# Kernel tuning notes

Hardware: AMD Instinct MI355X
Metric: run time of the kernel (lower is better)

The kernel has to match this reference:

```python
import jax, jax.numpy as jnp
import numpy as np

N_NODES = 50000
N_EDGES = 800000
IN_DIM = 128
HEADS = 8
HEAD_DIM = 16


def setup_inputs() -> dict:
    key = jax.random.key(0)
    ks = jax.random.split(key, 9)
    s = 1.0 / np.sqrt(IN_DIM)
    return {
        "h": jax.random.normal(ks[0], (N_NODES, IN_DIM), dtype=jnp.float32),
        "src": jax.random.randint(ks[1], (N_EDGES,), 0, N_NODES, dtype=jnp.int32),
        "dst": jax.random.randint(ks[2], (N_EDGES,), 0, N_NODES, dtype=jnp.int32),
        "WQ": jax.random.normal(ks[3], (IN_DIM, HEADS * HEAD_DIM), dtype=jnp.float32) * s,
        "bQ": jnp.zeros((HEADS * HEAD_DIM,), dtype=jnp.float32),
        "WK": jax.random.normal(ks[4], (IN_DIM, HEADS * HEAD_DIM), dtype=jnp.float32) * s,
        "bK": jnp.zeros((HEADS * HEAD_DIM,), dtype=jnp.float32),
        "WV": jax.random.normal(ks[5], (IN_DIM, HEADS * HEAD_DIM), dtype=jnp.float32) * s,
        "bV": jnp.zeros((HEADS * HEAD_DIM,), dtype=jnp.float32),
    }


def reference(h, src, dst, WQ, bQ, WK, bK, WV, bV):
    N = h.shape[0]
    sqrt_d = jnp.float32(np.sqrt(HEAD_DIM))
    # node projections, viewed as [N, H, D]
    Q = (h @ WQ + bQ).reshape(N, HEADS, HEAD_DIM)
    K = (h @ WK + bK).reshape(N, HEADS, HEAD_DIM)
    V = (h @ WV + bV).reshape(N, HEADS, HEAD_DIM)
    # edge scores: (K_src . Q_dst) per head, scaled exp with clamp [-5, 5]
    score = jnp.sum(K[src] * Q[dst], axis=-1, keepdims=True)  # [E, H, 1]
    score = jnp.exp(jnp.clip(score / sqrt_d, -5.0, 5.0))
    # segment-softmax denominator z and weighted V sum wV, both scattered to dst
    z = jax.ops.segment_sum(score, dst, num_segments=N)            # [N, H, 1]
    wV = jax.ops.segment_sum(V[src] * score, dst, num_segments=N)  # [N, H, D]
    # possible_empty: divide only where z > 0 (wV is 0 there anyway)
    head_out = jnp.where(z > 0, wV / jnp.where(z > 0, z, 1.0), wV)
    return head_out
```

## Files before the change

### kernel.cpp

```cpp
#include <hip/hip_runtime.h>
#include <math.h>

#define DIM 128
#define N_HEADS 8
#define HD 16

typedef __attribute__((ext_vector_type(8))) short bf16x8;
typedef __attribute__((ext_vector_type(4))) float f32x4;

__device__ __forceinline__ unsigned bf16pack2(float a, float b) {
    unsigned ua = __builtin_bit_cast(unsigned, a);
    unsigned ub = __builtin_bit_cast(unsigned, b);
    ua = (ua + 0x7FFFu + ((ua >> 16) & 1u)) >> 16;
    ub = (ub + 0x7FFFu + ((ub >> 16) & 1u)) >> 16;
    return ua | (ub << 16);
}
__device__ __forceinline__ float bf16lo(unsigned p) {
    return __builtin_bit_cast(float, p << 16);
}
__device__ __forceinline__ float bf16hi(unsigned p) {
    return __builtin_bit_cast(float, p & 0xFFFF0000u);
}

__global__ __launch_bounds__(256)
void convert_hist_kernel(const float* __restrict__ WQ, const float* __restrict__ bQ,
                         const float* __restrict__ WK, const float* __restrict__ bK,
                         const float* __restrict__ WV, const float* __restrict__ bV,
                         unsigned short* __restrict__ WT, float* __restrict__ bias384,
                         const int* __restrict__ dst, int* __restrict__ offs,
                         int nConv, int E)
{
    if ((int)blockIdx.x < nConv) {
        int idx = blockIdx.x * 256 + threadIdx.x;
        int c = idx >> 7, k = idx & 127;
        const float* W; const float* b; int col = c & 127;
        if (c < 128)      { W = WQ; b = bQ; }
        else if (c < 256) { W = WK; b = bK; }
        else              { W = WV; b = bV; }
        float v = W[k * DIM + col];
        WT[(size_t)c * DIM + k] = (unsigned short)(bf16pack2(v, 0.0f) & 0xFFFFu);
        if (k == 0) bias384[c] = b[col];
    } else {
        int e = ((int)blockIdx.x - nConv) * 256 + threadIdx.x;
        if (e < E) atomicAdd(&offs[dst[e]], 1);
    }
}

__global__ __launch_bounds__(256)
void scan_blocks_kernel(int* __restrict__ offs, int* __restrict__ bsum, int N)
{
    __shared__ int sd[256];
    const int t = threadIdx.x;
    const int i = blockIdx.x * 256 + t;
    int v = (i < N) ? offs[i] : 0;
    sd[t] = v;
    __syncthreads();
    #pragma unroll
    for (int o = 1; o < 256; o <<= 1) {
        int x = (t >= o) ? sd[t - o] : 0;
        __syncthreads();
        sd[t] += x;
        __syncthreads();
    }
    int incl = sd[t];
    if (i < N) offs[i] = incl - v;
    if (t == 255) bsum[blockIdx.x] = incl;
}

__global__ __launch_bounds__(256)
void scan_fixup_kernel(int* __restrict__ offs, int* __restrict__ cursor,
                       const int* __restrict__ bsum, int nb, int N, int E)
{
    __shared__ int sd[256];
    const int t = threadIdx.x;
    sd[t] = (t < nb && t < (int)blockIdx.x) ? bsum[t] : 0;
    __syncthreads();
    #pragma unroll
    for (int o = 128; o > 0; o >>= 1) {
        if (t < o) sd[t] += sd[t + o];
        __syncthreads();
    }
    const int base = sd[0];
    int i = blockIdx.x * 256 + t;
    if (i < N) {
        int v = offs[i] + base;
        offs[i]   = v;
        cursor[i] = v;
    }
    if (i == 0) offs[N] = E;
}

__global__ __launch_bounds__(256)
void scatter_kernel(const int* __restrict__ src, const int* __restrict__ dst,
                    int* __restrict__ cursor, int* __restrict__ srcs, int E)
{
    int e = blockIdx.x * 256 + threadIdx.x;
    if (e < E) {
        int d   = dst[e];
        int pos = atomicAdd(&cursor[d], 1);
        srcs[pos] = src[e];
    }
}

__global__ __launch_bounds__(256)
void qkv_mfma_kernel(const float* __restrict__ h,
                     const unsigned short* __restrict__ WT,
                     const float* __restrict__ bias384,
                     float* __restrict__ Q, unsigned* __restrict__ KVd,
                     int N)
{
    __shared__ unsigned short hs[64 * 136];
    const int tid = threadIdx.x;
    const int n0  = blockIdx.x * 64;

    #pragma unroll
    for (int i = 0; i < 4; ++i) {
        int lin  = i * 256 + tid;
        int node = lin >> 4;
        int k0   = (lin & 15) * 8;
        int gn   = n0 + node;
        float4 a0, a1;
        if (gn < N) {
            a0 = *(const float4*)(h + (size_t)gn * DIM + k0);
            a1 = *(const float4*)(h + (size_t)gn * DIM + k0 + 4);
        } else {
            a0 = make_float4(0.f, 0.f, 0.f, 0.f);
            a1 = a0;
        }
        uint4 p = make_uint4(bf16pack2(a0.x, a0.y), bf16pack2(a0.z, a0.w),
                             bf16pack2(a1.x, a1.y), bf16pack2(a1.z, a1.w));
        *(uint4*)(hs + node * 136 + k0) = p;
    }
    __syncthreads();

    const int wave   = tid >> 6;
    const int l      = tid & 63;
    const int lane16 = l & 15;
    const int quad   = l >> 4;
    const int wc0    = wave * 96;

    f32x4 acc[6][4];
    #pragma unroll
    for (int ct = 0; ct < 6; ++ct) {
        float4 bv = *(const float4*)(bias384 + wc0 + ct * 16 + quad * 4);
        #pragma unroll
        for (int rt = 0; rt < 4; ++rt)
            acc[ct][rt] = (f32x4){bv.x, bv.y, bv.z, bv.w};
    }

    #pragma unroll
    for (int ks = 0; ks < 4; ++ks) {
        bf16x8 a[6], b[4];
        #pragma unroll
        for (int ct = 0; ct < 6; ++ct)
            a[ct] = *(const bf16x8*)(WT + (size_t)(wc0 + ct * 16 + lane16) * DIM
                                         + ks * 32 + quad * 8);
        #pragma unroll
        for (int rt = 0; rt < 4; ++rt)
            b[rt] = *(const bf16x8*)(hs + (rt * 16 + lane16) * 136 + ks * 32 + quad * 8);
        #pragma unroll
        for (int ct = 0; ct < 6; ++ct)
            #pragma unroll
            for (int rt = 0; rt < 4; ++rt)
                acc[ct][rt] = __builtin_amdgcn_mfma_f32_16x16x32_bf16(
                    a[ct], b[rt], acc[ct][rt], 0, 0, 0);
    }

    #pragma unroll
    for (int ct = 0; ct < 6; ++ct) {
        const int col = wc0 + ct * 16 + quad * 4;
        #pragma unroll
        for (int rt = 0; rt < 4; ++rt) {
            int gn = n0 + rt * 16 + lane16;
            if (gn >= N) continue;
            f32x4 v = acc[ct][rt];
            if (col < 128) {
                *(float4*)(Q + (size_t)gn * DIM + col) =
                    make_float4(v[0], v[1], v[2], v[3]);
            } else if (col < 256) {
                int c = col - 128;
                KVd[(size_t)gn * 128 + c]     = bf16pack2(v[0], v[1]);
                KVd[(size_t)gn * 128 + c + 2] = bf16pack2(v[2], v[3]);
            } else {
                int c = col - 256;
                KVd[(size_t)gn * 128 + c + 1] = bf16pack2(v[0], v[1]);
                KVd[(size_t)gn * 128 + c + 3] = bf16pack2(v[2], v[3]);
            }
        }
    }
}

__device__ __forceinline__ void agg_step(uint2 kv, float2 q,
                                         float& ax, float& ay, float& zs)
{
    float p = bf16lo(kv.x) * q.x + bf16hi(kv.x) * q.y;
    p += __shfl_xor(p, 4);
    p += __shfl_xor(p, 2);
    p += __shfl_xor(p, 1);
    p = fminf(fmaxf(p * 0.25f, -5.0f), 5.0f);
    float w = __expf(p);
    ax += w * bf16lo(kv.y);
    ay += w * bf16hi(kv.y);
    zs += w;
}

__global__ __launch_bounds__(256)
void aggregate_kernel(const int* __restrict__ offs, const int* __restrict__ srcs,
                      const float* __restrict__ Q, const unsigned* __restrict__ KVd,
                      float* __restrict__ out, int N)
{
    const int node = blockIdx.x * 4 + (threadIdx.x >> 6);
    if (node >= N) return;
    const int l = threadIdx.x & 63;

    const float2 q = *(const float2*)(Q + (size_t)node * DIM + 2 * l);
    const int start = offs[node];
    const int end   = offs[node + 1];

    float ax = 0.0f, ay = 0.0f, zs = 0.0f;

    int e = start;
    for (; e + 8 <= end; e += 8) {
        uint2 kv[8];
        #pragma unroll
        for (int j = 0; j < 8; ++j) {
            int s = srcs[e + j];
            kv[j] = *(const uint2*)(KVd + (size_t)s * 128 + 2 * l);
        }
        float p[8];
        #pragma unroll
        for (int j = 0; j < 8; ++j)
            p[j] = bf16lo(kv[j].x) * q.x + bf16hi(kv[j].x) * q.y;
        #pragma unroll
        for (int j = 0; j < 8; ++j) p[j] += __shfl_xor(p[j], 4);
        #pragma unroll
        for (int j = 0; j < 8; ++j) p[j] += __shfl_xor(p[j], 2);
        #pragma unroll
        for (int j = 0; j < 8; ++j) p[j] += __shfl_xor(p[j], 1);
        #pragma unroll
        for (int j = 0; j < 8; ++j) {
            float pc = fminf(fmaxf(p[j] * 0.25f, -5.0f), 5.0f);
            float w  = __expf(pc);
            ax += w * bf16lo(kv[j].y);
            ay += w * bf16hi(kv[j].y);
            zs += w;
        }
    }
    for (; e + 4 <= end; e += 4) {
        uint2 kv[4];
        #pragma unroll
        for (int j = 0; j < 4; ++j) {
            int s = srcs[e + j];
            kv[j] = *(const uint2*)(KVd + (size_t)s * 128 + 2 * l);
        }
        float p[4];
        #pragma unroll
        for (int j = 0; j < 4; ++j)
            p[j] = bf16lo(kv[j].x) * q.x + bf16hi(kv[j].x) * q.y;
        #pragma unroll
        for (int j = 0; j < 4; ++j) p[j] += __shfl_xor(p[j], 4);
        #pragma unroll
        for (int j = 0; j < 4; ++j) p[j] += __shfl_xor(p[j], 2);
        #pragma unroll
        for (int j = 0; j < 4; ++j) p[j] += __shfl_xor(p[j], 1);
        #pragma unroll
        for (int j = 0; j < 4; ++j) {
            float pc = fminf(fmaxf(p[j] * 0.25f, -5.0f), 5.0f);
            float w  = __expf(pc);
            ax += w * bf16lo(kv[j].y);
            ay += w * bf16hi(kv[j].y);
            zs += w;
        }
    }
    for (; e < end; ++e) {
        int s0 = srcs[e];
        uint2 kv0 = *(const uint2*)(KVd + (size_t)s0 * 128 + 2 * l);
        agg_step(kv0, q, ax, ay, zs);
    }

    float inv = (zs > 0.0f) ? (1.0f / zs) : 0.0f;
    *(float2*)(out + (size_t)node * DIM + 2 * l) = make_float2(ax * inv, ay * inv);
}

extern "C" void kernel_launch(void* const* d_in, const int* in_sizes, int n_in,
                              void* d_out, int out_size, void* d_ws, size_t ws_size,
                              hipStream_t stream) {
    const float* h   = (const float*)d_in[0];
    const int*   src = (const int*)  d_in[1];
    const int*   dst = (const int*)  d_in[2];
    const float* WQ  = (const float*)d_in[3];
    const float* bQ  = (const float*)d_in[4];
    const float* WK  = (const float*)d_in[5];
    const float* bK  = (const float*)d_in[6];
    const float* WV  = (const float*)d_in[7];
    const float* bV  = (const float*)d_in[8];
    float* out = (float*)d_out;

    const int N  = in_sizes[0] / DIM;
    const int E  = in_sizes[1];
    const int NB = (N + 255) / 256;
    const int EB = (E + 255) / 256;
    const int nConv = (384 * DIM) / 256;

    char* w = (char*)d_ws;
    float*          Q       = (float*)w;           w += (size_t)N * DIM * sizeof(float);
    unsigned*       KVd     = (unsigned*)w;        w += (size_t)N * 128 * sizeof(unsigned);
    unsigned short* WT      = (unsigned short*)w;  w += (size_t)384 * DIM * sizeof(unsigned short);
    float*          bias384 = (float*)w;           w += 384 * sizeof(float);
    int*            offs    = (int*)w;             w += (size_t)(N + 1) * sizeof(int);
    int*            cursor  = (int*)w;             w += (size_t)N * sizeof(int);
    int*            bsum    = (int*)w;             w += 256 * sizeof(int);
    int*            srcs    = (int*)w;

    hipMemsetAsync(offs, 0, (size_t)(N + 1) * sizeof(int), stream);

    convert_hist_kernel<<<nConv + EB, 256, 0, stream>>>(WQ, bQ, WK, bK, WV, bV,
                                                        WT, bias384, dst, offs,
                                                        nConv, E);
    scan_blocks_kernel<<<NB, 256, 0, stream>>>(offs, bsum, N);
    scan_fixup_kernel<<<NB, 256, 0, stream>>>(offs, cursor, bsum, NB, N, E);
    scatter_kernel<<<EB, 256, 0, stream>>>(src, dst, cursor, srcs, E);
    qkv_mfma_kernel<<<(N + 63) / 64, 256, 0, stream>>>(h, WT, bias384, Q, KVd, N);
    aggregate_kernel<<<(N + 3) / 4, 256, 0, stream>>>(offs, srcs, Q, KVd, out, N);
}
```

Baseline: 263.4 us.

## Repack K/V in 8-element chunks and process four edges per wavefront in parallel

```diff
diff --git a/kernel.cpp b/kernel.cpp
--- a/kernel.cpp
+++ b/kernel.cpp
@@ -179,29 +179,17 @@
                     make_float4(v[0], v[1], v[2], v[3]);
             } else if (col < 256) {
                 int c = col - 128;
-                KVd[(size_t)gn * 128 + c]     = bf16pack2(v[0], v[1]);
-                KVd[(size_t)gn * 128 + c + 2] = bf16pack2(v[2], v[3]);
+                size_t base = (size_t)gn * 128 + ((c >> 3) * 8) + ((c & 4) >> 1);
+                KVd[base]     = bf16pack2(v[0], v[1]);
+                KVd[base + 1] = bf16pack2(v[2], v[3]);
             } else {
                 int c = col - 256;
-                KVd[(size_t)gn * 128 + c + 1] = bf16pack2(v[0], v[1]);
-                KVd[(size_t)gn * 128 + c + 3] = bf16pack2(v[2], v[3]);
+                size_t base = (size_t)gn * 128 + ((c >> 3) * 8) + 4 + ((c & 4) >> 1);
+                KVd[base]     = bf16pack2(v[0], v[1]);
+                KVd[base + 1] = bf16pack2(v[2], v[3]);
             }
         }
     }
-}
-
-__device__ __forceinline__ void agg_step(uint2 kv, float2 q,
-                                         float& ax, float& ay, float& zs)
-{
-    float p = bf16lo(kv.x) * q.x + bf16hi(kv.x) * q.y;
-    p += __shfl_xor(p, 4);
-    p += __shfl_xor(p, 2);
-    p += __shfl_xor(p, 1);
-    p = fminf(fmaxf(p * 0.25f, -5.0f), 5.0f);
-    float w = __expf(p);
-    ax += w * bf16lo(kv.y);
-    ay += w * bf16hi(kv.y);
-    zs += w;
 }
 
 __global__ __launch_bounds__(256)
@@ -211,75 +199,88 @@
 {
     const int node = blockIdx.x * 4 + (threadIdx.x >> 6);
     if (node >= N) return;
-    const int l = threadIdx.x & 63;
-
-    const float2 q = *(const float2*)(Q + (size_t)node * DIM + 2 * l);
+    const int l    = threadIdx.x & 63;
+    const int slot = l >> 4;
+    const int c    = l & 15;
+
+    const float4 qa = *(const float4*)(Q + (size_t)node * DIM + c * 8);
+    const float4 qb = *(const float4*)(Q + (size_t)node * DIM + c * 8 + 4);
+
     const int start = offs[node];
     const int end   = offs[node + 1];
 
-    float ax = 0.0f, ay = 0.0f, zs = 0.0f;
+    float acc[8] = {0.f, 0.f, 0.f, 0.f, 0.f, 0.f, 0.f, 0.f};
+    float zs = 0.f;
 
     int e = start;
     for (; e + 8 <= end; e += 8) {
-        uint2 kv[8];
-        #pragma unroll
-        for (int j = 0; j < 8; ++j) {
-            int s = srcs[e + j];
-            kv[j] = *(const uint2*)(KVd + (size_t)s * 128 + 2 * l);
-        }
-        float p[8];
-        #pragma unroll
-        for (int j = 0; j < 8; ++j)
-            p[j] = bf16lo(kv[j].x) * q.x + bf16hi(kv[j].x) * q.y;
-        #pragma unroll
-        for (int j = 0; j < 8; ++j) p[j] += __shfl_xor(p[j], 4);
-        #pragma unroll
-        for (int j = 0; j < 8; ++j) p[j] += __shfl_xor(p[j], 2);
-        #pragma unroll
-        for (int j = 0; j < 8; ++j) p[j] += __shfl_xor(p[j], 1);
-        #pragma unroll
-        for (int j = 0; j < 8; ++j) {
-            float pc = fminf(fmaxf(p[j] * 0.25f, -5.0f), 5.0f);
-            float w  = __expf(pc);
-            ax += w * bf16lo(kv[j].y);
-            ay += w * bf16hi(kv[j].y);
-            zs += w;
-        }
-    }
-    for (; e + 4 <= end; e += 4) {
-        uint2 kv[4];
-        #pragma unroll
-        for (int j = 0; j < 4; ++j) {
-            int s = srcs[e + j];
-            kv[j] = *(const uint2*)(KVd + (size_t)s * 128 + 2 * l);
-        }
-        float p[4];
-        #pragma unroll
-        for (int j = 0; j < 4; ++j)
-            p[j] = bf16lo(kv[j].x) * q.x + bf16hi(kv[j].x) * q.y;
-        #pragma unroll
-        for (int j = 0; j < 4; ++j) p[j] += __shfl_xor(p[j], 4);
-        #pragma unroll
-        for (int j = 0; j < 4; ++j) p[j] += __shfl_xor(p[j], 2);
-        #pragma unroll
-        for (int j = 0; j < 4; ++j) p[j] += __shfl_xor(p[j], 1);
-        #pragma unroll
-        for (int j = 0; j < 4; ++j) {
-            float pc = fminf(fmaxf(p[j] * 0.25f, -5.0f), 5.0f);
-            float w  = __expf(pc);
-            ax += w * bf16lo(kv[j].y);
-            ay += w * bf16hi(kv[j].y);
-            zs += w;
-        }
-    }
-    for (; e < end; ++e) {
-        int s0 = srcs[e];
-        uint2 kv0 = *(const uint2*)(KVd + (size_t)s0 * 128 + 2 * l);
-        agg_step(kv0, q, ax, ay, zs);
-    }
-
-    float inv = (zs > 0.0f) ? (1.0f / zs) : 0.0f;
-    *(float2*)(out + (size_t)node * DIM + 2 * l) = make_float2(ax * inv, ay * inv);
+        int s0 = srcs[e + slot];
+        int s1 = srcs[e + 4 + slot];
+        const uint4* p0 = (const uint4*)(KVd + (size_t)s0 * 128 + c * 8);
+        const uint4* p1 = (const uint4*)(KVd + (size_t)s1 * 128 + c * 8);
+        uint4 K0 = p0[0], V0 = p0[1];
+        uint4 K1 = p1[0], V1 = p1[1];
+
+        float d0 = bf16lo(K0.x) * qa.x + bf16hi(K0.x) * qa.y
+                 + bf16lo(K0.y) * qa.z + bf16hi(K0.y) * qa.w
+                 + bf16lo(K0.z) * qb.x + bf16hi(K0.z) * qb.y
+                 + bf16lo(K0.w) * qb.z + bf16hi(K0.w) * qb.w;
+        float d1 = bf16lo(K1.x) * qa.x + bf16hi(K1.x) * qa.y
+                 + bf16lo(K1.y) * qa.z + bf16hi(K1.y) * qa.w
+                 + bf16lo(K1.z) * qb.x + bf16hi(K1.z) * qb.y
+                 + bf16lo(K1.w) * qb.z + bf16hi(K1.w) * qb.w;
+        d0 += __shfl_xor(d0, 1);
+        d1 += __shfl_xor(d1, 1);
+        d0 = fminf(fmaxf(d0 * 0.25f, -5.0f), 5.0f);
+        d1 = fminf(fmaxf(d1 * 0.25f, -5.0f), 5.0f);
+        float w0 = __expf(d0);
+        float w1 = __expf(d1);
+        zs += w0 + w1;
+        acc[0] += w0 * bf16lo(V0.x); acc[1] += w0 * bf16hi(V0.x);
+        acc[2] += w0 * bf16lo(V0.y); acc[3] += w0 * bf16hi(V0.y);
+        acc[4] += w0 * bf16lo(V0.z); acc[5] += w0 * bf16hi(V0.z);
+        acc[6] += w0 * bf16lo(V0.w); acc[7] += w0 * bf16hi(V0.w);
+        acc[0] += w1 * bf16lo(V1.x); acc[1] += w1 * bf16hi(V1.x);
+        acc[2] += w1 * bf16lo(V1.y); acc[3] += w1 * bf16hi(V1.y);
+        acc[4] += w1 * bf16lo(V1.z); acc[5] += w1 * bf16hi(V1.z);
+        acc[6] += w1 * bf16lo(V1.w); acc[7] += w1 * bf16hi(V1.w);
+    }
+    for (; e < end; e += 4) {
+        int  eg    = e + slot;
+        bool valid = eg < end;
+        int  s0    = srcs[valid ? eg : (end - 1)];
+        const uint4* p0 = (const uint4*)(KVd + (size_t)s0 * 128 + c * 8);
+        uint4 K0 = p0[0], V0 = p0[1];
+
+        float d0 = bf16lo(K0.x) * qa.x + bf16hi(K0.x) * qa.y
+                 + bf16lo(K0.y) * qa.z + bf16hi(K0.y) * qa.w
+                 + bf16lo(K0.z) * qb.x + bf16hi(K0.z) * qb.y
+                 + bf16lo(K0.w) * qb.z + bf16hi(K0.w) * qb.w;
+        d0 += __shfl_xor(d0, 1);
+        d0 = fminf(fmaxf(d0 * 0.25f, -5.0f), 5.0f);
+        float w0 = valid ? __expf(d0) : 0.0f;
+        zs += w0;
+        acc[0] += w0 * bf16lo(V0.x); acc[1] += w0 * bf16hi(V0.x);
+        acc[2] += w0 * bf16lo(V0.y); acc[3] += w0 * bf16hi(V0.y);
+        acc[4] += w0 * bf16lo(V0.z); acc[5] += w0 * bf16hi(V0.z);
+        acc[6] += w0 * bf16lo(V0.w); acc[7] += w0 * bf16hi(V0.w);
+    }
+
+    #pragma unroll
+    for (int j = 0; j < 8; ++j) {
+        acc[j] += __shfl_xor(acc[j], 16);
+        acc[j] += __shfl_xor(acc[j], 32);
+    }
+    zs += __shfl_xor(zs, 16);
+    zs += __shfl_xor(zs, 32);
+
+    if (slot == 0) {
+        float inv = (zs > 0.0f) ? (1.0f / zs) : 0.0f;
+        *(float4*)(out + (size_t)node * DIM + c * 8) =
+            make_float4(acc[0] * inv, acc[1] * inv, acc[2] * inv, acc[3] * inv);
+        *(float4*)(out + (size_t)node * DIM + c * 8 + 4) =
+            make_float4(acc[4] * inv, acc[5] * inv, acc[6] * inv, acc[7] * inv);
+    }
 }
 
 extern "C" void kernel_launch(void* const* d_in, const int* in_sizes, int n_in,
```

New measurement: 265.0 us. No clear change (+0.6%).
